# Optimization experiments

Hardware: AMD Instinct MI355X
Metric: run time of the kernel (lower is better)

The kernel has to match this reference:

```python
import jax, jax.numpy as jnp
import numpy as np

B, T, I, H, O = 64, 2048, 128, 256, 128

def setup_inputs() -> dict:
    key = jax.random.key(0)
    ks = jax.random.split(key, 7)
    return {
        "x": jax.random.normal(ks[0], (B, T, I), dtype=jnp.float32),
        "Wi": jax.random.normal(ks[1], (H, I), dtype=jnp.float32) / np.sqrt(I),
        "bi": jax.random.normal(ks[2], (H,), dtype=jnp.float32) * 0.01,
        "Wh": jax.random.normal(ks[3], (H, H), dtype=jnp.float32) / np.sqrt(H),
        "bh": jax.random.normal(ks[4], (H,), dtype=jnp.float32) * 0.01,
        "Wo": jax.random.normal(ks[5], (O, H), dtype=jnp.float32) / np.sqrt(H),
        "bo": jax.random.normal(ks[6], (O,), dtype=jnp.float32) * 0.01,
    }

def reference(x, Wi, bi, Wh, bh, Wo, bo):
    # x: [B, T, I]; torch Linear weights are [out, in] -> right-multiply by W.T
    b = x.shape[0]
    h0 = jnp.zeros((b, Wh.shape[0]), dtype=x.dtype)
    # precompute input projection for all timesteps (batched GEMM)
    xproj = jnp.einsum('bti,hi->bth', x, Wi) + bi  # [B, T, H]

    def step(h, xp_t):
        h = jnp.tanh(xp_t + h @ Wh.T + bh)
        return h, h

    _, hs = jax.lax.scan(step, h0, jnp.swapaxes(xproj, 0, 1))  # hs: [T, B, H]
    hs = jnp.swapaxes(hs, 0, 1)  # [B, T, H]
    out = jnp.einsum('bth,oh->bto', hs, Wo) + bo  # [B, T, O]
    return out
```

## Files before the change

### kernel.cpp

```cpp
#include <hip/hip_runtime.h>
#include <hip/hip_bf16.h>

#define BB 64
#define TT 2048
#define II 128
#define HH 256
#define OO 128

typedef float f32x4v __attribute__((ext_vector_type(4)));
typedef short bf16x8 __attribute__((ext_vector_type(8)));
typedef unsigned short ushortv4 __attribute__((ext_vector_type(4)));

__device__ __forceinline__ float bf16bits_to_f32(unsigned short u) {
    return __uint_as_float((unsigned)u << 16);
}
__device__ __forceinline__ unsigned short f2bf(float f) {
    union { __hip_bfloat16 h; unsigned short u; } cv;
    cv.h = __float2bfloat16(f);
    return cv.u;
}
__device__ __forceinline__ float tanh_fast(float x) {
    float y = x * 2.88539008177793f;
    float e;
    asm("v_exp_f32 %0, %1" : "=v"(e) : "v"(y));
    return fmaf(-2.0f, __builtin_amdgcn_rcpf(e + 1.0f), 1.0f);
}


#define BM 64
#define BN 64
#define BKT 32

__global__ __launch_bounds__(256) void gemm_f32_bt(
    const float* __restrict__ A, const float* __restrict__ B,
    const float* __restrict__ bias, const float* __restrict__ bias2,
    float* __restrict__ C, int M, int N, int K)
{
    __shared__ __align__(16) float As[BKT][BM + 4];
    __shared__ __align__(16) float Bs[BKT][BN + 4];

    const int t  = threadIdx.x;
    const int m0 = blockIdx.x * BM;
    const int n0 = blockIdx.y * BN;
    const int r  = t >> 3;
    const int kq = (t & 7) * 4;
    const int tx = t & 15;
    const int ty = t >> 4;

    float acc[4][4] = {};

    for (int k0 = 0; k0 < K; k0 += BKT) {
        float4 a0 = *(const float4*)&A[(size_t)(m0 + r)      * K + k0 + kq];
        float4 a1 = *(const float4*)&A[(size_t)(m0 + r + 32) * K + k0 + kq];
        float4 b0 = *(const float4*)&B[(size_t)(n0 + r)      * K + k0 + kq];
        float4 b1 = *(const float4*)&B[(size_t)(n0 + r + 32) * K + k0 + kq];

        __syncthreads();
        As[kq + 0][r] = a0.x; As[kq + 1][r] = a0.y; As[kq + 2][r] = a0.z; As[kq + 3][r] = a0.w;
        As[kq + 0][r + 32] = a1.x; As[kq + 1][r + 32] = a1.y; As[kq + 2][r + 32] = a1.z; As[kq + 3][r + 32] = a1.w;
        Bs[kq + 0][r] = b0.x; Bs[kq + 1][r] = b0.y; Bs[kq + 2][r] = b0.z; Bs[kq + 3][r] = b0.w;
        Bs[kq + 0][r + 32] = b1.x; Bs[kq + 1][r + 32] = b1.y; Bs[kq + 2][r + 32] = b1.z; Bs[kq + 3][r + 32] = b1.w;
        __syncthreads();

#pragma unroll
        for (int k = 0; k < BKT; ++k) {
            float4 avv = *(const float4*)&As[k][ty * 4];
            float4 bvv = *(const float4*)&Bs[k][tx * 4];
            const float* av = &avv.x;
            const float* bv = &bvv.x;
#pragma unroll
            for (int i = 0; i < 4; ++i)
#pragma unroll
                for (int j = 0; j < 4; ++j)
                    acc[i][j] = fmaf(av[i], bv[j], acc[i][j]);
        }
    }

#pragma unroll
    for (int i = 0; i < 4; ++i) {
#pragma unroll
        for (int j = 0; j < 4; ++j) {
            const int c = n0 + tx * 4 + j;
            float v = acc[i][j] + bias[c] + bias2[c];
            const int pos = (c & ~31) + 2 * (c & 15) + ((c & 31) >> 4);
            C[(size_t)(m0 + ty * 4 + i) * N + pos] = v;
        }
    }
}

__global__ __launch_bounds__(256) void gemm_bf16a_bt(
    const unsigned short* __restrict__ A, const float* __restrict__ B,
    const float* __restrict__ bias, float* __restrict__ C,
    int M, int N, int K)
{
    __shared__ __align__(16) float As[BKT][BM + 4];
    __shared__ __align__(16) float Bs[BKT][BN + 4];

    const int t  = threadIdx.x;
    const int m0 = blockIdx.x * BM;
    const int n0 = blockIdx.y * BN;
    const int r  = t >> 3;
    const int kq = (t & 7) * 4;
    const int kh = kq >> 1;
    const int tx = t & 15;
    const int ty = t >> 4;

    float acc[4][4] = {};

    for (int k0 = 0; k0 < K; k0 += BKT) {
        ushortv4 a0 = *(const ushortv4*)&A[(size_t)(m0 + r)      * K + k0 + kq];
        ushortv4 a1 = *(const ushortv4*)&A[(size_t)(m0 + r + 32) * K + k0 + kq];
        float4  b0 = *(const float4*)&B[(size_t)(n0 + r)      * K + k0 + kq];
        float4  b1 = *(const float4*)&B[(size_t)(n0 + r + 32) * K + k0 + kq];

        __syncthreads();
        As[kh + 0][r]  = bf16bits_to_f32(a0[0]); As[kh + 16][r] = bf16bits_to_f32(a0[1]);
        As[kh + 1][r]  = bf16bits_to_f32(a0[2]); As[kh + 17][r] = bf16bits_to_f32(a0[3]);
        As[kh + 0][r + 32]  = bf16bits_to_f32(a1[0]); As[kh + 16][r + 32] = bf16bits_to_f32(a1[1]);
        As[kh + 1][r + 32]  = bf16bits_to_f32(a1[2]); As[kh + 17][r + 32] = bf16bits_to_f32(a1[3]);
        Bs[kq + 0][r] = b0.x; Bs[kq + 1][r] = b0.y; Bs[kq + 2][r] = b0.z; Bs[kq + 3][r] = b0.w;
        Bs[kq + 0][r + 32] = b1.x; Bs[kq + 1][r + 32] = b1.y; Bs[kq + 2][r + 32] = b1.z; Bs[kq + 3][r + 32] = b1.w;
        __syncthreads();

#pragma unroll
        for (int k = 0; k < BKT; ++k) {
            float4 avv = *(const float4*)&As[k][ty * 4];
            float4 bvv = *(const float4*)&Bs[k][tx * 4];
            const float* av = &avv.x;
            const float* bv = &bvv.x;
#pragma unroll
            for (int i = 0; i < 4; ++i)
#pragma unroll
                for (int j = 0; j < 4; ++j)
                    acc[i][j] = fmaf(av[i], bv[j], acc[i][j]);
        }
    }

#pragma unroll
    for (int i = 0; i < 4; ++i) {
        float4 o;
        o.x = acc[i][0] + bias[n0 + tx * 4 + 0];
        o.y = acc[i][1] + bias[n0 + tx * 4 + 1];
        o.z = acc[i][2] + bias[n0 + tx * 4 + 2];
        o.w = acc[i][3] + bias[n0 + tx * 4 + 3];
        *(float4*)&C[(size_t)(m0 + ty * 4 + i) * N + n0 + tx * 4] = o;
    }
}

#define G 16
#define HPAD 264

__global__ __launch_bounds__(512) __attribute__((amdgpu_waves_per_eu(2, 2)))
void rnn_recurrence_mfma(
    const float* __restrict__ xproj, const float* __restrict__ Wh,
    unsigned short* __restrict__ hs)
{
    __shared__ __align__(16) unsigned short hbl[2][G][HPAD];

    const int blk  = blockIdx.x;
    const int tid  = threadIdx.x;
    const int wave = tid >> 6;
    const int lane = tid & 63;
    const int l15  = lane & 15;
    const int lg   = lane >> 4;
    const int n0   = wave * 32;

#define LOADB(nt, kt, dst) { \
        const float* wp = Wh + (size_t)(n0 + (nt)*16 + l15) * HH + (kt)*32 + lg*4; \
        dst[0] = (short)f2bf(wp[0]);  dst[1] = (short)f2bf(wp[16]); \
        dst[2] = (short)f2bf(wp[1]);  dst[3] = (short)f2bf(wp[17]); \
        dst[4] = (short)f2bf(wp[2]);  dst[5] = (short)f2bf(wp[18]); \
        dst[6] = (short)f2bf(wp[3]);  dst[7] = (short)f2bf(wp[19]); }

    bf16x8 B00, B01, B02, B03, B04, B05, B06, B07;
    bf16x8 B10, B11, B12, B13, B14, B15, B16, B17;
    LOADB(0, 0, B00) LOADB(0, 1, B01) LOADB(0, 2, B02) LOADB(0, 3, B03)
    LOADB(0, 4, B04) LOADB(0, 5, B05) LOADB(0, 6, B06) LOADB(0, 7, B07)
    LOADB(1, 0, B10) LOADB(1, 1, B11) LOADB(1, 2, B12) LOADB(1, 3, B13)
    LOADB(1, 4, B14) LOADB(1, 5, B15) LOADB(1, 6, B16) LOADB(1, 7, B17)

    const int mb = blk * G + lg * 4;
    const float* xq0 = xproj + (size_t)(mb + 0) * TT * HH + n0 + 2 * l15;
    const float* xq1 = xproj + (size_t)(mb + 1) * TT * HH + n0 + 2 * l15;
    const float* xq2 = xproj + (size_t)(mb + 2) * TT * HH + n0 + 2 * l15;
    const float* xq3 = xproj + (size_t)(mb + 3) * TT * HH + n0 + 2 * l15;
    unsigned short* hq0 = hs + (size_t)(mb + 0) * TT * HH + n0 + 2 * l15 - HH;
    unsigned short* hq1 = hs + (size_t)(mb + 1) * TT * HH + n0 + 2 * l15 - HH;
    unsigned short* hq2 = hs + (size_t)(mb + 2) * TT * HH + n0 + 2 * l15 - HH;
    unsigned short* hq3 = hs + (size_t)(mb + 3) * TT * HH + n0 + 2 * l15 - HH;

    for (int i = tid; i < G * HPAD / 2; i += 512)
        ((unsigned int*)hbl[0])[i] = 0u;
    float2 xvA0 = *(const float2*)xq0;
    float2 xvA1 = *(const float2*)xq1;
    float2 xvA2 = *(const float2*)xq2;
    float2 xvA3 = *(const float2*)xq3;
    float2 xvB0, xvB1, xvB2, xvB3;
    unsigned int svA0 = 0, svA1 = 0, svA2 = 0, svA3 = 0;
    unsigned int svB0 = 0, svB1 = 0, svB2 = 0, svB3 = 0;
    __syncthreads();

#define MM(a, b, c) c = __builtin_amdgcn_mfma_f32_16x16x32_bf16(a, b, c, 0, 0, 0);
#define STEP(P, XC, XN, SVST, SVNEW, COND, LOFF, SOFF) { \
    const unsigned short* hrow = &hbl[P][l15][lg * 8]; \
    bf16x8 a0 = *(const bf16x8*)(hrow + 0 * 32); \
    bf16x8 a1 = *(const bf16x8*)(hrow + 1 * 32); \
    bf16x8 a2 = *(const bf16x8*)(hrow + 2 * 32); \
    bf16x8 a3 = *(const bf16x8*)(hrow + 3 * 32); \
    bf16x8 a4 = *(const bf16x8*)(hrow + 4 * 32); \
    bf16x8 a5 = *(const bf16x8*)(hrow + 5 * 32); \
    bf16x8 a6 = *(const bf16x8*)(hrow + 6 * 32); \
    bf16x8 a7 = *(const bf16x8*)(hrow + 7 * 32); \
    XN##0 = *(const float2*)((const char*)xq0 + (LOFF)); \
    XN##1 = *(const float2*)((const char*)xq1 + (LOFF)); \
    XN##2 = *(const float2*)((const char*)xq2 + (LOFF)); \
    XN##3 = *(const float2*)((const char*)xq3 + (LOFF)); \
    if (COND) { \
        *(unsigned int*)((char*)hq0 + (SOFF)) = SVST##0; \
        *(unsigned int*)((char*)hq1 + (SOFF)) = SVST##1; \
        *(unsigned int*)((char*)hq2 + (SOFF)) = SVST##2; \
        *(unsigned int*)((char*)hq3 + (SOFF)) = SVST##3; \
    } \
    f32x4v c0 = {(XC##0).x, (XC##1).x, (XC##2).x, (XC##3).x}; \
    f32x4v c1 = {(XC##0).y, (XC##1).y, (XC##2).y, (XC##3).y}; \
    MM(a0, B00, c0) MM(a0, B10, c1) \
    MM(a1, B01, c0) MM(a1, B11, c1) \
    MM(a2, B02, c0) MM(a2, B12, c1) \
    MM(a3, B03, c0) MM(a3, B13, c1) \
    MM(a4, B04, c0) MM(a4, B14, c1) \
    MM(a5, B05, c0) MM(a5, B15, c1) \
    MM(a6, B06, c0) MM(a6, B16, c1) \
    MM(a7, B07, c0) MM(a7, B17, c1) \
    { float h0 = tanh_fast(c0[0]); float h1 = tanh_fast(c1[0]); \
      asm("v_cvt_pk_bf16_f32 %0, %1, %2" : "=v"(SVNEW##0) : "v"(h0), "v"(h1)); \
      *(unsigned int*)&hbl[(P) ^ 1][lg * 4 + 0][n0 + 2 * l15] = SVNEW##0; } \
    { float h0 = tanh_fast(c0[1]); float h1 = tanh_fast(c1[1]); \
      asm("v_cvt_pk_bf16_f32 %0, %1, %2" : "=v"(SVNEW##1) : "v"(h0), "v"(h1)); \
      *(unsigned int*)&hbl[(P) ^ 1][lg * 4 + 1][n0 + 2 * l15] = SVNEW##1; } \
    { float h0 = tanh_fast(c0[2]); float h1 = tanh_fast(c1[2]); \
      asm("v_cvt_pk_bf16_f32 %0, %1, %2" : "=v"(SVNEW##2) : "v"(h0), "v"(h1)); \
      *(unsigned int*)&hbl[(P) ^ 1][lg * 4 + 2][n0 + 2 * l15] = SVNEW##2; } \
    { float h0 = tanh_fast(c0[3]); float h1 = tanh_fast(c1[3]); \
      asm("v_cvt_pk_bf16_f32 %0, %1, %2" : "=v"(SVNEW##3) : "v"(h0), "v"(h1)); \
      *(unsigned int*)&hbl[(P) ^ 1][lg * 4 + 3][n0 + 2 * l15] = SVNEW##3; } \
    __builtin_amdgcn_sched_barrier(0); \
    asm volatile("s_waitcnt lgkmcnt(0)" ::: "memory"); \
    __builtin_amdgcn_s_barrier(); \
    asm volatile("" ::: "memory"); \
    __builtin_amdgcn_sched_barrier(0); \
}

    for (int t = 0; t < TT; t += 2) {
        STEP(0, xvA, xvB, svB, svA, (t != 0), HH * 4, 0)
        STEP(1, xvB, xvA, svA, svB, 1, HH * 8, HH * 2)
        xq0 += 2 * HH; xq1 += 2 * HH; xq2 += 2 * HH; xq3 += 2 * HH;
        hq0 += 2 * HH; hq1 += 2 * HH; hq2 += 2 * HH; hq3 += 2 * HH;
    }

    *(unsigned int*)hq0 = svB0;
    *(unsigned int*)hq1 = svB1;
    *(unsigned int*)hq2 = svB2;
    *(unsigned int*)hq3 = svB3;
}

extern "C" void kernel_launch(void* const* d_in, const int* in_sizes, int n_in,
                              void* d_out, int out_size, void* d_ws, size_t ws_size,
                              hipStream_t stream)
{
    const float* x  = (const float*)d_in[0];
    const float* Wi = (const float*)d_in[1];
    const float* bi = (const float*)d_in[2];
    const float* Wh = (const float*)d_in[3];
    const float* bh = (const float*)d_in[4];
    const float* Wo = (const float*)d_in[5];
    const float* bo = (const float*)d_in[6];
    float* out = (float*)d_out;

    const int M = BB * TT;

    float* xproj = (float*)d_ws;
    unsigned short* hs = (unsigned short*)((char*)d_ws + (size_t)M * HH * sizeof(float));

    gemm_f32_bt<<<dim3(M / BM, HH / BN), 256, 0, stream>>>(x, Wi, bi, bh, xproj, M, HH, II);

    rnn_recurrence_mfma<<<dim3(4), 512, 0, stream>>>(xproj, Wh, hs);

    gemm_bf16a_bt<<<dim3(M / BM, OO / BN), 256, 0, stream>>>(
        hs, Wo, bo, out, M, OO, HH);
}
```

Before: 1.514 ms.

## Transpose xproj layout for vector loads and use rational tanh in recurrence

The input-projection GEMM now writes xproj in a batch-interleaved layout, blocked as [batch group][t][h][16 batches]. Each recurrence lane can then load its four batch accumulator rows with one 16-byte vector load instead of four scattered float2 loads. tanh changes from an exp plus reciprocal to a polynomial rational (Pade) approximation that shares one reciprocal across four values using packed float2 math. The hand-written waitcnt/barrier sequence is replaced by __syncthreads, and the loads and stores are reordered. The GEMM store becomes strided with a 16-float stride, which may make that kernel slower, and the Pade approximation is unclamped, so it may lose accuracy for large inputs.

```diff
diff --git a/kernel.cpp b/kernel.cpp
--- a/kernel.cpp
+++ b/kernel.cpp
@@ -7,6 +7,7 @@
 #define HH 256
 #define OO 128
 
+typedef float f32x2 __attribute__((ext_vector_type(2)));
 typedef float f32x4v __attribute__((ext_vector_type(4)));
 typedef short bf16x8 __attribute__((ext_vector_type(8)));
 typedef unsigned short ushortv4 __attribute__((ext_vector_type(4)));
@@ -19,12 +20,44 @@
     cv.h = __float2bfloat16(f);
     return cv.u;
 }
-__device__ __forceinline__ float tanh_fast(float x) {
-    float y = x * 2.88539008177793f;
-    float e;
-    asm("v_exp_f32 %0, %1" : "=v"(e) : "v"(y));
-    return fmaf(-2.0f, __builtin_amdgcn_rcpf(e + 1.0f), 1.0f);
-}
+
+#define PA1  4.89352455891786e-03f
+#define PA3  6.37261928875436e-04f
+#define PA5  1.48572235717979e-05f
+#define PA7  5.12229709037114e-08f
+#define PA9  -8.60467152213735e-11f
+#define PA11 2.00018790482477e-13f
+#define PA13 -2.76076847742355e-16f
+#define QB0  4.89352518554385e-03f
+#define QB2  2.26843463243900e-03f
+#define QB4  1.18534705686654e-04f
+#define QB6  1.19825839466702e-06f
+
+__device__ __forceinline__ void pade_nd(f32x2 x, f32x2* n, f32x2* d) {
+    f32x2 z = x * x;
+    f32x2 p = {PA13, PA13};
+    p = p * z + PA11;
+    p = p * z + PA9;
+    p = p * z + PA7;
+    p = p * z + PA5;
+    p = p * z + PA3;
+    p = p * z + PA1;
+    *n = p * x;
+    f32x2 q = {QB6, QB6};
+    q = q * z + QB4;
+    q = q * z + QB2;
+    q = q * z + QB0;
+    *d = q;
+}
+
+#define TANH4(xA, xB, o0, o1, o2, o3) { \
+    f32x2 nA, dA, nB, dB; \
+    pade_nd(xA, &nA, &dA); pade_nd(xB, &nB, &dB); \
+    float t1 = dA.x * dA.y, t2 = dB.x * dB.y; \
+    float r = __builtin_amdgcn_rcpf(t1 * t2); \
+    float rA = r * t2, rB = r * t1; \
+    o0 = nA.x * dA.y * rA; o1 = nA.y * dA.x * rA; \
+    o2 = nB.x * dB.y * rB; o3 = nB.y * dB.x * rB; }
 
 
 #define BM 64
@@ -34,7 +67,7 @@
 __global__ __launch_bounds__(256) void gemm_f32_bt(
     const float* __restrict__ A, const float* __restrict__ B,
     const float* __restrict__ bias, const float* __restrict__ bias2,
-    float* __restrict__ C, int M, int N, int K)
+    float* __restrict__ CT, int M, int N, int K)
 {
     __shared__ __align__(16) float As[BKT][BM + 4];
     __shared__ __align__(16) float Bs[BKT][BN + 4];
@@ -78,12 +111,15 @@
 
 #pragma unroll
     for (int i = 0; i < 4; ++i) {
+        const int mg = m0 + ty * 4 + i;
+        const int bb = mg >> 11;
+        const int tt = mg & 2047;
 #pragma unroll
         for (int j = 0; j < 4; ++j) {
             const int c = n0 + tx * 4 + j;
             float v = acc[i][j] + bias[c] + bias2[c];
             const int pos = (c & ~31) + 2 * (c & 15) + ((c & 31) >> 4);
-            C[(size_t)(m0 + ty * 4 + i) * N + pos] = v;
+            CT[(((size_t)(bb >> 4) * TT + tt) * HH + pos) * 16 + (bb & 15)] = v;
         }
     }
 }
@@ -152,7 +188,7 @@
 
 __global__ __launch_bounds__(512) __attribute__((amdgpu_waves_per_eu(2, 2)))
 void rnn_recurrence_mfma(
-    const float* __restrict__ xproj, const float* __restrict__ Wh,
+    const float* __restrict__ xprojT, const float* __restrict__ Wh,
     unsigned short* __restrict__ hs)
 {
     __shared__ __align__(16) unsigned short hbl[2][G][HPAD];
@@ -179,11 +215,9 @@
     LOADB(1, 0, B10) LOADB(1, 1, B11) LOADB(1, 2, B12) LOADB(1, 3, B13)
     LOADB(1, 4, B14) LOADB(1, 5, B15) LOADB(1, 6, B16) LOADB(1, 7, B17)
 
+    const float* xT = xprojT + (((size_t)blk * TT + 0) * HH + (n0 + 2 * l15)) * 16 + lg * 4;
+
     const int mb = blk * G + lg * 4;
-    const float* xq0 = xproj + (size_t)(mb + 0) * TT * HH + n0 + 2 * l15;
-    const float* xq1 = xproj + (size_t)(mb + 1) * TT * HH + n0 + 2 * l15;
-    const float* xq2 = xproj + (size_t)(mb + 2) * TT * HH + n0 + 2 * l15;
-    const float* xq3 = xproj + (size_t)(mb + 3) * TT * HH + n0 + 2 * l15;
     unsigned short* hq0 = hs + (size_t)(mb + 0) * TT * HH + n0 + 2 * l15 - HH;
     unsigned short* hq1 = hs + (size_t)(mb + 1) * TT * HH + n0 + 2 * l15 - HH;
     unsigned short* hq2 = hs + (size_t)(mb + 2) * TT * HH + n0 + 2 * l15 - HH;
@@ -191,17 +225,24 @@
 
     for (int i = tid; i < G * HPAD / 2; i += 512)
         ((unsigned int*)hbl[0])[i] = 0u;
-    float2 xvA0 = *(const float2*)xq0;
-    float2 xvA1 = *(const float2*)xq1;
-    float2 xvA2 = *(const float2*)xq2;
-    float2 xvA3 = *(const float2*)xq3;
-    float2 xvB0, xvB1, xvB2, xvB3;
+    f32x4v xA0 = *(const f32x4v*)xT;
+    f32x4v xA1 = *(const f32x4v*)(xT + 16);
+    f32x4v xB0, xB1;
     unsigned int svA0 = 0, svA1 = 0, svA2 = 0, svA3 = 0;
     unsigned int svB0 = 0, svB1 = 0, svB2 = 0, svB3 = 0;
     __syncthreads();
 
 #define MM(a, b, c) c = __builtin_amdgcn_mfma_f32_16x16x32_bf16(a, b, c, 0, 0, 0);
-#define STEP(P, XC, XN, SVST, SVNEW, COND, LOFF, SOFF) { \
+#define STEP(P, XC0, XC1, XN0, XN1, SVST, SVNEW, COND, SOFF) { \
+    if (COND) { \
+        *(unsigned int*)((char*)hq0 + (SOFF)) = SVST##0; \
+        *(unsigned int*)((char*)hq1 + (SOFF)) = SVST##1; \
+        *(unsigned int*)((char*)hq2 + (SOFF)) = SVST##2; \
+        *(unsigned int*)((char*)hq3 + (SOFF)) = SVST##3; \
+    } \
+    xT += (size_t)HH * 16;                  \
+    XN0 = *(const f32x4v*)xT; \
+    XN1 = *(const f32x4v*)(xT + 16); \
     const unsigned short* hrow = &hbl[P][l15][lg * 8]; \
     bf16x8 a0 = *(const bf16x8*)(hrow + 0 * 32); \
     bf16x8 a1 = *(const bf16x8*)(hrow + 1 * 32); \
@@ -211,18 +252,8 @@
     bf16x8 a5 = *(const bf16x8*)(hrow + 5 * 32); \
     bf16x8 a6 = *(const bf16x8*)(hrow + 6 * 32); \
     bf16x8 a7 = *(const bf16x8*)(hrow + 7 * 32); \
-    XN##0 = *(const float2*)((const char*)xq0 + (LOFF)); \
-    XN##1 = *(const float2*)((const char*)xq1 + (LOFF)); \
-    XN##2 = *(const float2*)((const char*)xq2 + (LOFF)); \
-    XN##3 = *(const float2*)((const char*)xq3 + (LOFF)); \
-    if (COND) { \
-        *(unsigned int*)((char*)hq0 + (SOFF)) = SVST##0; \
-        *(unsigned int*)((char*)hq1 + (SOFF)) = SVST##1; \
-        *(unsigned int*)((char*)hq2 + (SOFF)) = SVST##2; \
-        *(unsigned int*)((char*)hq3 + (SOFF)) = SVST##3; \
-    } \
-    f32x4v c0 = {(XC##0).x, (XC##1).x, (XC##2).x, (XC##3).x}; \
-    f32x4v c1 = {(XC##0).y, (XC##1).y, (XC##2).y, (XC##3).y}; \
+    f32x4v c0 = XC0; \
+    f32x4v c1 = XC1; \
     MM(a0, B00, c0) MM(a0, B10, c1) \
     MM(a1, B01, c0) MM(a1, B11, c1) \
     MM(a2, B02, c0) MM(a2, B12, c1) \
@@ -231,29 +262,25 @@
     MM(a5, B05, c0) MM(a5, B15, c1) \
     MM(a6, B06, c0) MM(a6, B16, c1) \
     MM(a7, B07, c0) MM(a7, B17, c1) \
-    { float h0 = tanh_fast(c0[0]); float h1 = tanh_fast(c1[0]); \
-      asm("v_cvt_pk_bf16_f32 %0, %1, %2" : "=v"(SVNEW##0) : "v"(h0), "v"(h1)); \
-      *(unsigned int*)&hbl[(P) ^ 1][lg * 4 + 0][n0 + 2 * l15] = SVNEW##0; } \
-    { float h0 = tanh_fast(c0[1]); float h1 = tanh_fast(c1[1]); \
-      asm("v_cvt_pk_bf16_f32 %0, %1, %2" : "=v"(SVNEW##1) : "v"(h0), "v"(h1)); \
-      *(unsigned int*)&hbl[(P) ^ 1][lg * 4 + 1][n0 + 2 * l15] = SVNEW##1; } \
-    { float h0 = tanh_fast(c0[2]); float h1 = tanh_fast(c1[2]); \
-      asm("v_cvt_pk_bf16_f32 %0, %1, %2" : "=v"(SVNEW##2) : "v"(h0), "v"(h1)); \
-      *(unsigned int*)&hbl[(P) ^ 1][lg * 4 + 2][n0 + 2 * l15] = SVNEW##2; } \
-    { float h0 = tanh_fast(c0[3]); float h1 = tanh_fast(c1[3]); \
-      asm("v_cvt_pk_bf16_f32 %0, %1, %2" : "=v"(SVNEW##3) : "v"(h0), "v"(h1)); \
-      *(unsigned int*)&hbl[(P) ^ 1][lg * 4 + 3][n0 + 2 * l15] = SVNEW##3; } \
-    __builtin_amdgcn_sched_barrier(0); \
-    asm volatile("s_waitcnt lgkmcnt(0)" ::: "memory"); \
-    __builtin_amdgcn_s_barrier(); \
-    asm volatile("" ::: "memory"); \
-    __builtin_amdgcn_sched_barrier(0); \
+    f32x2 pA = {c0[0], c0[1]}, pB = {c0[2], c0[3]}; \
+    f32x2 pC = {c1[0], c1[1]}, pD = {c1[2], c1[3]}; \
+    float th0, th1, th2, th3, th4, th5, th6, th7; \
+    TANH4(pA, pB, th0, th1, th2, th3) \
+    TANH4(pC, pD, th4, th5, th6, th7) \
+    asm("v_cvt_pk_bf16_f32 %0, %1, %2" : "=v"(SVNEW##0) : "v"(th0), "v"(th4)); \
+    asm("v_cvt_pk_bf16_f32 %0, %1, %2" : "=v"(SVNEW##1) : "v"(th1), "v"(th5)); \
+    asm("v_cvt_pk_bf16_f32 %0, %1, %2" : "=v"(SVNEW##2) : "v"(th2), "v"(th6)); \
+    asm("v_cvt_pk_bf16_f32 %0, %1, %2" : "=v"(SVNEW##3) : "v"(th3), "v"(th7)); \
+    *(unsigned int*)&hbl[(P) ^ 1][lg * 4 + 0][n0 + 2 * l15] = SVNEW##0; \
+    *(unsigned int*)&hbl[(P) ^ 1][lg * 4 + 1][n0 + 2 * l15] = SVNEW##1; \
+    *(unsigned int*)&hbl[(P) ^ 1][lg * 4 + 2][n0 + 2 * l15] = SVNEW##2; \
+    *(unsigned int*)&hbl[(P) ^ 1][lg * 4 + 3][n0 + 2 * l15] = SVNEW##3; \
+    __syncthreads(); \
 }
 
     for (int t = 0; t < TT; t += 2) {
-        STEP(0, xvA, xvB, svB, svA, (t != 0), HH * 4, 0)
-        STEP(1, xvB, xvA, svA, svB, 1, HH * 8, HH * 2)
-        xq0 += 2 * HH; xq1 += 2 * HH; xq2 += 2 * HH; xq3 += 2 * HH;
+        STEP(0, xA0, xA1, xB0, xB1, svB, svA, (t != 0), 0)
+        STEP(1, xB0, xB1, xA0, xA1, svA, svB, 1, HH * 2)
         hq0 += 2 * HH; hq1 += 2 * HH; hq2 += 2 * HH; hq3 += 2 * HH;
     }
 
@@ -278,12 +305,12 @@
 
     const int M = BB * TT;
 
-    float* xproj = (float*)d_ws;
+    float* xprojT = (float*)d_ws;
     unsigned short* hs = (unsigned short*)((char*)d_ws + (size_t)M * HH * sizeof(float));
 
-    gemm_f32_bt<<<dim3(M / BM, HH / BN), 256, 0, stream>>>(x, Wi, bi, bh, xproj, M, HH, II);
-
-    rnn_recurrence_mfma<<<dim3(4), 512, 0, stream>>>(xproj, Wh, hs);
+    gemm_f32_bt<<<dim3(M / BM, HH / BN), 256, 0, stream>>>(x, Wi, bi, bh, xprojT, M, HH, II);
+
+    rnn_recurrence_mfma<<<dim3(4), 512, 0, stream>>>(xprojT, Wh, hs);
 
     gemm_bf16a_bt<<<dim3(M / BM, OO / BN), 256, 0, stream>>>(
         hs, Wo, bo, out, M, OO, HH);
```

Result: slower. 2.114 ms (+39.7%).
